# Kernel tuning notes

Hardware: AMD Instinct MI355X
Metric: run time of the kernel (lower is better)

The kernel has to match this reference:

```python
import jax, jax.numpy as jnp
import numpy as np

MAX_DISP = 48


def setup_inputs() -> dict:
    key = jax.random.key(0)
    k1, k2 = jax.random.split(key)
    left = jax.random.normal(k1, (2, 64, 256, 32), dtype=jnp.float32)
    right = jax.random.normal(k2, (2, 64, 256, 32), dtype=jnp.float32)
    return {"left": left, "right": right}


def reference(left, right):
    # left, right: [B, H, W, C] NHWC feature maps.
    # For each disparity d in [-D, D): out[b, d+D, h, w] = concat(left[b,h,w], right[b,h,w-d])
    # where positions with (w - d) out of [0, W) are zeroed (matches TF concat+pad semantics:
    # the pad zeroes BOTH the left and right channel halves in the invalid region).
    B, H, W, C = left.shape
    disps = jnp.arange(-MAX_DISP, MAX_DISP)          # [2D]
    w_idx = jnp.arange(W)                            # [W]

    def level(d):
        idx = w_idx - d                              # right-image column for each output column
        valid = (idx >= 0) & (idx < W)               # [W]
        r = jnp.take(right, jnp.clip(idx, 0, W - 1), axis=2)   # [B,H,W,C]
        lvl = jnp.concatenate([left, r], axis=-1)               # [B,H,W,2C]
        return jnp.where(valid[None, None, :, None], lvl, jnp.zeros((), lvl.dtype))

    cv = jax.vmap(level)(disps)                      # [2D, B, H, W, 2C]
    return jnp.transpose(cv, (1, 0, 2, 3, 4))        # [B, 2D, H, W, 2C]
```

## Files before the change

### kernel.cpp

```cpp
#include <hip/hip_runtime.h>


typedef float f4 __attribute__((ext_vector_type(4)));

#define DD_STRIDE 262144

__global__ __launch_bounds__(256) void cost_concat_kernel(
    const f4* __restrict__ left4,
    const f4* __restrict__ right4,
    f4* __restrict__ out4)
{
    __shared__ f4 lds[4096];

    const int t   = threadIdx.x;
    const int blk = blockIdx.x;
    const int g   = blk & 3;
    const int hb  = blk >> 2;
    const int rowBase = hb * 2048;

    #pragma unroll
    for (int k = 0; k < 8; ++k)
        lds[k * 256 + t] = left4[rowBase + k * 256 + t];
    #pragma unroll
    for (int k = 0; k < 8; ++k)
        lds[2048 + k * 256 + t] = right4[rowBase + k * 256 + t];
    __syncthreads();

    const int c4  = t & 15;
    const int wb  = t >> 4;
    const bool isLeft = c4 < 8;
    const int cc  = c4 & 7;
    const int b   = hb >> 6;
    const int h   = hb & 63;
    const int dd0 = g * 24;

    f4* orow = out4 + (size_t)b * 25165824 + (size_t)dd0 * DD_STRIDE + (size_t)h * 4096;

    for (int k = 0; k < 24; ++k) {
        const int d = dd0 + k - 48;
        f4* op = orow + (size_t)k * DD_STRIDE + t;
        #pragma unroll
        for (int j = 0; j < 16; ++j) {
            const int w   = j * 16 + wb;
            const int idx = w - d;
            const bool valid = (unsigned)idx < 256u;
            const int ci  = valid ? idx : 0;
            const int la  = isLeft ? (w * 8 + cc) : (2048 + ci * 8 + cc);
            f4 v = lds[la];
            v = valid ? v : (f4){0.f, 0.f, 0.f, 0.f};
            op[j * 256] = v;
        }
    }
}

extern "C" void kernel_launch(void* const* d_in, const int* in_sizes, int n_in,
                              void* d_out, int out_size, void* d_ws, size_t ws_size,
                              hipStream_t stream) {
    const f4* left4  = (const f4*)d_in[0];
    const f4* right4 = (const f4*)d_in[1];
    f4* out4 = (f4*)d_out;

    cost_concat_kernel<<<512, 256, 0, stream>>>(left4, right4, out4);
}
```

Measured before the change: 148.9 us.

## Split cost-volume work by width half, shrink LDS, use nontemporal stores

Blocks now each handle half the image width and half the disparities (48 each) instead of a quarter of the disparities over full width. Only the needed right-image window, padded with zeros, is staged in LDS, so less shared memory is used per block. The inner loop uses strength-reduced byte addresses and a zero slot instead of per-element select logic. Output writes use nontemporal stores to avoid polluting the cache. The grid stays at 512 blocks, so per-block work and total traffic are unchanged.

Measured after the change: 155.0 us. 4.1% more time.

```diff
diff --git a/kernel.cpp b/kernel.cpp
--- a/kernel.cpp
+++ b/kernel.cpp
@@ -10,46 +10,60 @@
     const f4* __restrict__ right4,
     f4* __restrict__ out4)
 {
-    __shared__ f4 lds[4096];
+    __shared__ f4 lds[2824];
 
     const int t   = threadIdx.x;
-    const int blk = blockIdx.x;
-    const int g   = blk & 3;
-    const int hb  = blk >> 2;
+    const int bid = blockIdx.x;
+    const int g   = bid & 1;
+    const int wh  = (bid >> 1) & 1;
+    const int hb  = bid >> 2;
+    const int w0  = wh << 7;
+    const int dd0 = g * 48;
     const int rowBase = hb * 2048;
 
     #pragma unroll
-    for (int k = 0; k < 8; ++k)
-        lds[k * 256 + t] = left4[rowBase + k * 256 + t];
+    for (int k = 0; k < 4; ++k)
+        lds[k * 256 + t] = left4[rowBase + w0 * 8 + k * 256 + t];
+
     #pragma unroll
-    for (int k = 0; k < 8; ++k)
-        lds[2048 + k * 256 + t] = right4[rowBase + k * 256 + t];
+    for (int k = 0; k < 7; ++k) {
+        const int q = k * 256 + t;
+        const int idxPix = (w0 - 48) + (q >> 3);
+        f4 v = (f4){0.f, 0.f, 0.f, 0.f};
+        if ((unsigned)idxPix < 256u)
+            v = right4[rowBase + idxPix * 8 + (q & 7)];
+        lds[1024 + q] = v;
+    }
+    if (t < 8) lds[2816 + t] = (f4){0.f, 0.f, 0.f, 0.f};
     __syncthreads();
 
-    const int c4  = t & 15;
-    const int wb  = t >> 4;
+    const int c4 = t & 15;
+    const int wb = t >> 4;
+    const int cc = c4 & 7;
     const bool isLeft = c4 < 8;
-    const int cc  = c4 & 7;
-    const int b   = hb >> 6;
-    const int h   = hb & 63;
-    const int dd0 = g * 24;
 
-    f4* orow = out4 + (size_t)b * 25165824 + (size_t)dd0 * DD_STRIDE + (size_t)h * 4096;
+    const int Z = 2816 * 16;
+    int addrB = isLeft ? (wb * 128 + cc * 16)
+                       : (16384 + (wb - dd0 + 96) * 128 + cc * 16);
+    const int dec = isLeft ? 0 : 128;
+    int ib = w0 + wb + 48 - dd0;
 
-    for (int k = 0; k < 24; ++k) {
-        const int d = dd0 + k - 48;
-        f4* op = orow + (size_t)k * DD_STRIDE + t;
+    const int b = hb >> 6, h = hb & 63;
+    f4* op = out4 + (size_t)b * 25165824 + (size_t)dd0 * DD_STRIDE
+                  + (size_t)h * 4096 + (size_t)(w0 * 16) + t;
+
+    const char* ldsb = (const char*)lds;
+
+    for (int k = 0; k < 48; ++k) {
         #pragma unroll
-        for (int j = 0; j < 16; ++j) {
-            const int w   = j * 16 + wb;
-            const int idx = w - d;
-            const bool valid = (unsigned)idx < 256u;
-            const int ci  = valid ? idx : 0;
-            const int la  = isLeft ? (w * 8 + cc) : (2048 + ci * 8 + cc);
-            f4 v = lds[la];
-            v = valid ? v : (f4){0.f, 0.f, 0.f, 0.f};
-            op[j * 256] = v;
+        for (int j = 0; j < 8; ++j) {
+            const int idxj = ib + j * 16;
+            const int aj   = addrB + j * 2048;
+            const int sel  = ((unsigned)idxj < 256u) ? aj : Z;
+            f4 v = *(const f4*)(ldsb + sel);
+            __builtin_nontemporal_store(v, op + j * 256);
         }
+        ib -= 1; addrB -= dec; op += DD_STRIDE;
     }
 }
 
```

## Split waves into left/right halves, keep left in registers, double grid

Applied to the files above, without the earlier changes.

Each block now handles 12 disparities instead of 24, which doubles the grid to 1024 blocks. Waves are split so half write the left channel half straight from registers, with no LDS reads and a simple zero mask. The other half read the right channels from LDS and fetch zeros from a padded zero slot instead of using a select. LDS use drops by half, and the extra blocks should give more occupancy and better write throughput, at the cost of reloading the input rows twice as often and having wave-divergent roles.

Result: slower. 158.0 us (+6.1%).

```diff
diff --git a/kernel.cpp b/kernel.cpp
--- a/kernel.cpp
+++ b/kernel.cpp
@@ -10,45 +10,63 @@
     const f4* __restrict__ right4,
     f4* __restrict__ out4)
 {
-    __shared__ f4 lds[4096];
+    __shared__ f4 ldsR[2056];
 
     const int t   = threadIdx.x;
-    const int blk = blockIdx.x;
-    const int g   = blk & 3;
-    const int hb  = blk >> 2;
+    const int bid = blockIdx.x;
+    const int g   = bid & 7;
+    const int hb  = bid >> 3;
+    const int dd0 = g * 12;
     const int rowBase = hb * 2048;
 
     #pragma unroll
-    for (int k = 0; k < 8; ++k)
-        lds[k * 256 + t] = left4[rowBase + k * 256 + t];
-    #pragma unroll
-    for (int k = 0; k < 8; ++k)
-        lds[2048 + k * 256 + t] = right4[rowBase + k * 256 + t];
+    for (int i = 0; i < 8; ++i)
+        ldsR[i * 256 + t] = right4[rowBase + i * 256 + t];
+    if (t < 8) ldsR[2048 + t] = (f4){0.f, 0.f, 0.f, 0.f};
+
+    const int lane = t & 63;
+    const int wv   = t >> 6;
+    const int s    = wv & 1;
+    const int pg   = wv >> 1;
+    const int cc   = lane & 7;
+    const int px   = pg * 8 + (lane >> 3);
+
+    f4 Lreg[16];
+    if (s == 0) {
+        #pragma unroll
+        for (int j = 0; j < 16; ++j)
+            Lreg[j] = left4[rowBase + (j * 16 + px) * 8 + cc];
+    }
+
     __syncthreads();
 
-    const int c4  = t & 15;
-    const int wb  = t >> 4;
-    const bool isLeft = c4 < 8;
-    const int cc  = c4 & 7;
-    const int b   = hb >> 6;
-    const int h   = hb & 63;
-    const int dd0 = g * 24;
+    const int b = hb >> 6, h = hb & 63;
+    f4* op0 = out4 + (size_t)b * 25165824 + (size_t)dd0 * DD_STRIDE
+                   + (size_t)h * 4096 + (size_t)(px * 16 + s * 8 + cc);
+    const f4 z = (f4){0.f, 0.f, 0.f, 0.f};
 
-    f4* orow = out4 + (size_t)b * 25165824 + (size_t)dd0 * DD_STRIDE + (size_t)h * 4096;
-
-    for (int k = 0; k < 24; ++k) {
-        const int d = dd0 + k - 48;
-        f4* op = orow + (size_t)k * DD_STRIDE + t;
-        #pragma unroll
-        for (int j = 0; j < 16; ++j) {
-            const int w   = j * 16 + wb;
-            const int idx = w - d;
-            const bool valid = (unsigned)idx < 256u;
-            const int ci  = valid ? idx : 0;
-            const int la  = isLeft ? (w * 8 + cc) : (2048 + ci * 8 + cc);
-            f4 v = lds[la];
-            v = valid ? v : (f4){0.f, 0.f, 0.f, 0.f};
-            op[j * 256] = v;
+    if (s == 0) {
+        for (int k = 0; k < 12; ++k) {
+            const int d = dd0 + k - 48;
+            f4* op = op0 + (size_t)k * DD_STRIDE;
+            #pragma unroll
+            for (int j = 0; j < 16; ++j) {
+                const int w = j * 16 + px;
+                const bool valid = (unsigned)(w - d) < 256u;
+                op[j * 256] = valid ? Lreg[j] : z;
+            }
+        }
+    } else {
+        for (int k = 0; k < 12; ++k) {
+            const int d = dd0 + k - 48;
+            f4* op = op0 + (size_t)k * DD_STRIDE;
+            #pragma unroll
+            for (int j = 0; j < 16; ++j) {
+                const int idx = j * 16 + px - d;
+                const bool valid = (unsigned)idx < 256u;
+                const int la = valid ? (idx * 8 + cc) : (2048 + cc);
+                op[j * 256] = ldsR[la];
+            }
         }
     }
 }
@@ -60,5 +78,5 @@
     const f4* right4 = (const f4*)d_in[1];
     f4* out4 = (f4*)d_out;
 
-    cost_concat_kernel<<<512, 256, 0, stream>>>(left4, right4, out4);
+    cost_concat_kernel<<<1024, 256, 0, stream>>>(left4, right4, out4);
 }
```

## Retile cost-volume kernel by width chunk and interleaved disparities with zero-pad LDS

Applied to the files above, without the earlier changes.

Each block now covers a 64-column chunk of one row and a residue class of disparities (stride 4), looping over both batches. It stages only the needed left slice and a halo-extended right window in LDS, with an explicit zero slot, so invalid positions become a branch-free address select. Grid and block size double (1024x512), and per-iteration address arithmetic is reduced to simple decrements. The aim is a leaner, more uniform store loop and higher occupancy for this write-bound kernel. The cost is a more intricate index mapping and an extra barrier between the two batch passes.

Measured after the change: 179.8 us. 20.7% more time.

```diff
diff --git a/kernel.cpp b/kernel.cpp
--- a/kernel.cpp
+++ b/kernel.cpp
@@ -3,52 +3,66 @@
 
 typedef float f4 __attribute__((ext_vector_type(4)));
 
-#define DD_STRIDE 262144
-
-__global__ __launch_bounds__(256) void cost_concat_kernel(
+__global__ __launch_bounds__(512) void cost_concat_kernel(
     const f4* __restrict__ left4,
     const f4* __restrict__ right4,
     f4* __restrict__ out4)
 {
-    __shared__ f4 lds[4096];
+    __shared__ f4 lds[1768];
 
-    const int t   = threadIdx.x;
-    const int blk = blockIdx.x;
-    const int g   = blk & 3;
-    const int hb  = blk >> 2;
-    const int rowBase = hb * 2048;
+    const int t  = threadIdx.x;
+    const int i  = blockIdx.x;
+    const int wc = i & 3;
+    const int h  = (i >> 2) & 63;
+    const int r0 = i >> 8;
+    const int w0 = wc << 6;
+    const int idx_lo = w0 - r0 - 44;
 
-    #pragma unroll
-    for (int k = 0; k < 8; ++k)
-        lds[k * 256 + t] = left4[rowBase + k * 256 + t];
-    #pragma unroll
-    for (int k = 0; k < 8; ++k)
-        lds[2048 + k * 256 + t] = right4[rowBase + k * 256 + t];
-    __syncthreads();
+    const int c4 = t & 15;
+    const int tb = t >> 4;
+    const int cc = c4 & 7;
+    const bool isLeft = c4 < 8;
+    const int Z = 28160;
 
-    const int c4  = t & 15;
-    const int wb  = t >> 4;
-    const bool isLeft = c4 < 8;
-    const int cc  = c4 & 7;
-    const int b   = hb >> 6;
-    const int h   = hb & 63;
-    const int dd0 = g * 24;
+    const char* lb = (const char*)lds;
+    f4* op = out4 + (size_t)i * 1024 + t;
 
-    f4* orow = out4 + (size_t)b * 25165824 + (size_t)dd0 * DD_STRIDE + (size_t)h * 4096;
+    for (int b = 0; b < 2; ++b) {
+        const int rowBase = (b * 64 + h) * 2048;
+        if (b) __syncthreads();
 
-    for (int k = 0; k < 24; ++k) {
-        const int d = dd0 + k - 48;
-        f4* op = orow + (size_t)k * DD_STRIDE + t;
+        lds[t] = left4[rowBase + w0 * 8 + t];
         #pragma unroll
-        for (int j = 0; j < 16; ++j) {
-            const int w   = j * 16 + wb;
-            const int idx = w - d;
-            const bool valid = (unsigned)idx < 256u;
-            const int ci  = valid ? idx : 0;
-            const int la  = isLeft ? (w * 8 + cc) : (2048 + ci * 8 + cc);
-            f4 v = lds[la];
-            v = valid ? v : (f4){0.f, 0.f, 0.f, 0.f};
-            op[j * 256] = v;
+        for (int u = 0; u < 3; ++u) {
+            const int q = u * 512 + t;
+            if (q < 1248) {
+                const int col = idx_lo + (q >> 3);
+                f4 v = (f4){0.f, 0.f, 0.f, 0.f};
+                if ((unsigned)col < 256u) v = right4[rowBase + col * 8 + (q & 7)];
+                lds[512 + q] = v;
+            }
+        }
+        if (t < 8) lds[1760 + t] = (f4){0.f, 0.f, 0.f, 0.f};
+        __syncthreads();
+
+        int addr0 = isLeft ? ((tb * 8 + cc) * 16)
+                           : ((512 + (tb + 92) * 8 + cc) * 16);
+        int addr1 = isLeft ? (((32 + tb) * 8 + cc) * 16)
+                           : ((512 + (32 + tb + 92) * 8 + cc) * 16);
+        int iv0 = w0 + tb + 48 - r0;
+        int iv1 = iv0 + 32;
+        const int dec = isLeft ? 0 : 512;
+
+        for (int s2 = 0; s2 < 24; ++s2) {
+            const int sel0 = ((unsigned)iv0 < 256u) ? addr0 : Z;
+            const int sel1 = ((unsigned)iv1 < 256u) ? addr1 : Z;
+            f4 v0 = *(const f4*)(lb + sel0);
+            f4 v1 = *(const f4*)(lb + sel1);
+            op[0]   = v0;
+            op[512] = v1;
+            iv0 -= 4; iv1 -= 4;
+            addr0 -= dec; addr1 -= dec;
+            op += 1048576;
         }
     }
 }
@@ -60,5 +74,5 @@
     const f4* right4 = (const f4*)d_in[1];
     f4* out4 = (f4*)d_out;
 
-    cost_concat_kernel<<<512, 256, 0, stream>>>(left4, right4, out4);
+    cost_concat_kernel<<<1024, 512, 0, stream>>>(left4, right4, out4);
 }
```
